# Kernel tuning notes

Measured on AMD Instinct MI355X. Metric: run time of the kernel, lower is better.

## Reference

```python
import jax, jax.numpy as jnp
import numpy as np

B, N, C = 32, 577, 768
H = 12
DH = C // H  # 64
SCALE = DH ** -0.5


def setup_inputs() -> dict:
    key = jax.random.key(0)
    ks = jax.random.split(key, 5)
    x = jax.random.normal(ks[0], (B, N, C), dtype=jnp.float32)
    # Linear params (torch convention: y = x @ W.T + b)
    qkv_w = jax.random.normal(ks[1], (3 * C, C), dtype=jnp.float32) * (C ** -0.5)
    qkv_b = jnp.zeros((3 * C,), dtype=jnp.float32)
    proj_w = jax.random.normal(ks[2], (C, C), dtype=jnp.float32) * (C ** -0.5)
    proj_b = jnp.zeros((C,), dtype=jnp.float32)
    return {"x": x, "qkv_w": qkv_w, "qkv_b": qkv_b, "proj_w": proj_w, "proj_b": proj_b}


def reference(x, qkv_w, qkv_b, proj_w, proj_b):
    b, n, c = x.shape
    qkv = x @ qkv_w.T + qkv_b                       # [B, N, 3C]
    qkv = qkv.reshape(b, n, 3, H, DH).transpose(2, 0, 3, 1, 4)  # [3, B, H, N, DH]
    q, k, v = qkv[0], qkv[1], qkv[2]
    q = q * SCALE
    attn = jnp.einsum('bhnd,bhmd->bhnm', q, k)      # [B, H, N, N]
    # sigmoid -> inverse-sigmoid straight-through rewrite (forward equals logit(sigmoid(attn)))
    sig = jax.nn.sigmoid(attn)
    inv_sig = jnp.log(sig / (1.0 - sig))
    attn_st = attn + jax.lax.stop_gradient(inv_sig - attn)
    p = jax.nn.softmax(attn_st, axis=-1)
    out = jnp.einsum('bhnm,bhmd->bhnd', p, v)       # [B, H, N, DH]
    out = out.transpose(0, 2, 1, 3).reshape(b, n, c)
    return out @ proj_w.T + proj_b
```

## Files before the change

kernel.cpp:

```cpp
#include <hip/hip_runtime.h>

typedef __bf16 bf16;
typedef __attribute__((ext_vector_type(4))) __bf16 bf16x4;
typedef __attribute__((ext_vector_type(8))) __bf16 bf16x8;
typedef __attribute__((ext_vector_type(4))) float f32x4;

#define MFMA_BF16(A_, B_, C_) __builtin_amdgcn_mfma_f32_16x16x32_bf16(A_, B_, C_, 0, 0, 0)

#define BB    32
#define SEQ   577
#define CH    768
#define NH    12
#define DHD   64
#define MROWS (BB * SEQ)
#define NQKV  2304
#define SEQP  584
#define QSCALE 0.1803368801111204f

__device__ __forceinline__ void async_ld16(const bf16* g, bf16* l) {
  __builtin_amdgcn_global_load_lds(
      (const __attribute__((address_space(1))) void*)g,
      (__attribute__((address_space(3))) void*)l, 16, 0, 0);
}

__global__ __launch_bounds__(256) void cvt_bf16(const float* __restrict__ src,
                                                bf16* __restrict__ dst, int n) {
  int idx = (blockIdx.x * 256 + threadIdx.x) * 4;
  if (idx >= n) return;
  float4 v = *(const float4*)(src + idx);
  bf16x4 o = {(bf16)v.x, (bf16)v.y, (bf16)v.z, (bf16)v.w};
  *(bf16x4*)(dst + idx) = o;
}

template <int EPI>
__global__ __launch_bounds__(256, 2)
void gemm_bt(const bf16* __restrict__ A, const bf16* __restrict__ W,
             const float* __restrict__ bias,
             bf16* __restrict__ qrm, bf16* __restrict__ krm, bf16* __restrict__ vt,
             float* __restrict__ out) {
  __shared__ bf16 As[2][128 * 32];
  __shared__ bf16 Bs[2][128 * 32];
  const int tid = threadIdx.x, lane = tid & 63, wid = tid >> 6;
  const int quad = lane >> 4, r15 = lane & 15;
  const int m0 = blockIdx.y * 128, n0 = blockIdx.x * 128;
  const int waveM = wid & 1, waveN = wid >> 1;

  const bf16* aSrc[2];
  const bf16* bSrc[2];
  for (int c = 0; c < 2; ++c) {
    int q = wid * 128 + c * 64 + lane;
    int row = q >> 2;
    int sw = (row ^ (row >> 2)) & 3;
    int kc = (q & 3) ^ sw;
    aSrc[c] = A + (size_t)(m0 + row) * CH + kc * 8;
    bSrc[c] = W + (size_t)(n0 + row) * CH + kc * 8;
  }

  f32x4 acc[4][4];
#pragma unroll
  for (int i = 0; i < 4; ++i)
#pragma unroll
    for (int j = 0; j < 4; ++j) acc[i][j] = (f32x4){0.f, 0.f, 0.f, 0.f};

#define GSTAGE(K0, BUF)                                                   \
  {                                                                       \
    _Pragma("unroll") for (int c = 0; c < 2; ++c) {                       \
      async_ld16(aSrc[c] + (K0), &As[BUF][(wid * 128 + c * 64) * 8]);     \
      async_ld16(bSrc[c] + (K0), &Bs[BUF][(wid * 128 + c * 64) * 8]);     \
    }                                                                     \
  }

#define GCOMPUTE(BUF)                                                     \
  {                                                                       \
    bf16x8 af[4], bfr[4];                                                 \
    _Pragma("unroll") for (int s = 0; s < 4; ++s) {                       \
      int rowA = waveM * 64 + s * 16 + r15;                               \
      int ca = quad ^ ((rowA ^ (rowA >> 2)) & 3);                         \
      af[s] = *(const bf16x8*)(&As[BUF][rowA * 32 + ca * 8]);             \
      int rowB = waveN * 64 + s * 16 + r15;                               \
      int cb = quad ^ ((rowB ^ (rowB >> 2)) & 3);                         \
      bfr[s] = *(const bf16x8*)(&Bs[BUF][rowB * 32 + cb * 8]);            \
    }                                                                     \
    _Pragma("unroll") for (int sm = 0; sm < 4; ++sm)                      \
      _Pragma("unroll") for (int sn = 0; sn < 4; ++sn)                    \
        acc[sm][sn] = MFMA_BF16(af[sm], bfr[sn], acc[sm][sn]);            \
  }

  GSTAGE(0, 0);
  for (int k0 = 0; k0 < CH; k0 += 64) {
    __syncthreads();
    GSTAGE(k0 + 32, 1);
    GCOMPUTE(0);
    __syncthreads();
    if (k0 + 64 < CH) GSTAGE(k0 + 64, 0);
    GCOMPUTE(1);
  }

  if (EPI == 0) {
    int t = (n0 >= 1536) ? 2 : (n0 >= 768 ? 1 : 0);
#pragma unroll
    for (int sn = 0; sn < 4; ++sn) {
      int gn = n0 + waveN * 64 + sn * 16 + r15;
      float bv = bias[gn];
      int col = gn - t * CH;
      int h = col >> 6, d = col & 63;
#pragma unroll
      for (int sm = 0; sm < 4; ++sm) {
        int gmBase = m0 + waveM * 64 + sm * 16 + quad * 4;
#pragma unroll
        for (int r = 0; r < 4; ++r) {
          int gm = gmBase + r;
          if (gm < MROWS) {
            float v = acc[sm][sn][r] + bv;
            if (t == 0) {
              qrm[(size_t)gm * CH + col] = (bf16)(v * QSCALE);
            } else if (t == 1) {
              krm[(size_t)gm * CH + col] = (bf16)v;
            } else {
              int b_ = gm / SEQ;
              int n_ = gm - b_ * SEQ;
              vt[((size_t)(b_ * NH + h) * DHD + d) * SEQP + n_] = (bf16)v;
            }
          }
        }
      }
    }
  } else {
#pragma unroll
    for (int sn = 0; sn < 4; ++sn) {
      int gn = n0 + waveN * 64 + sn * 16 + r15;
      float bv = bias[gn];
#pragma unroll
      for (int sm = 0; sm < 4; ++sm) {
        int gmBase = m0 + waveM * 64 + sm * 16 + quad * 4;
#pragma unroll
        for (int r = 0; r < 4; ++r) {
          int gm = gmBase + r;
          if (gm < MROWS) out[(size_t)gm * CH + gn] = acc[sm][sn][r] + bv;
        }
      }
    }
  }
}

__global__ __launch_bounds__(256, 6)
void attn_kernel(const bf16* __restrict__ qrm, const bf16* __restrict__ krm,
                 const bf16* __restrict__ vt, bf16* __restrict__ ob) {
  __shared__ bf16 Ks[64 * 72];
  __shared__ bf16 Vt[64 * 72];
  const int tid = threadIdx.x, lane = tid & 63, wid = tid >> 6;
  const int quad = lane >> 4, r15 = lane & 15;
  const int qt = blockIdx.x, bh = blockIdx.y;
  const int b_ = bh / NH, h = bh - b_ * NH;
  const bf16* vtb = vt + (size_t)bh * DHD * SEQP;

  int qrow = qt * 64 + wid * 16 + r15;
  if (qrow > SEQ - 1) qrow = SEQ - 1;
  const bf16* qp = qrm + (size_t)(b_ * SEQ + qrow) * CH + h * DHD + quad * 8;
  bf16x8 qf0 = *(const bf16x8*)qp;
  bf16x8 qf1 = *(const bf16x8*)(qp + 32);

  f32x4 oacc[4];
#pragma unroll
  for (int i = 0; i < 4; ++i) oacc[i] = (f32x4){0.f, 0.f, 0.f, 0.f};
  float lrow[4] = {0.f, 0.f, 0.f, 0.f};

  for (int j0 = 0; j0 < SEQ; j0 += 64) {
    __syncthreads();
#pragma unroll
    for (int c = 0; c < 2; ++c) {
      int sid = c * 256 + tid;
      int row = sid >> 3, cc = sid & 7;
      int jr = j0 + row;
      if (jr > SEQ - 1) jr = SEQ - 1;
      *(bf16x8*)(Ks + row * 72 + cc * 8) =
          *(const bf16x8*)(krm + (size_t)(b_ * SEQ + jr) * CH + h * DHD + cc * 8);
      int jst = j0 + cc * 8;
      if (jst > SEQ - 1) jst = SEQ - 1;
      *(bf16x8*)(Vt + row * 72 + cc * 8) = *(const bf16x8*)(vtb + (size_t)row * SEQP + jst);
    }
    __syncthreads();

    f32x4 s[4];
#pragma unroll
    for (int sj = 0; sj < 4; ++sj) {
      bf16x8 kf0 = *(const bf16x8*)(Ks + (sj * 16 + r15) * 72 + quad * 8);
      bf16x8 kf1 = *(const bf16x8*)(Ks + (sj * 16 + r15) * 72 + 32 + quad * 8);
      f32x4 z = (f32x4){0.f, 0.f, 0.f, 0.f};
      s[sj] = MFMA_BF16(qf0, kf0, z);
      s[sj] = MFMA_BF16(qf1, kf1, s[sj]);
    }
#pragma unroll
    for (int sj = 0; sj < 4; ++sj)
      if (j0 + sj * 16 + r15 > SEQ - 1) s[sj] = (f32x4){-1e30f, -1e30f, -1e30f, -1e30f};

#pragma unroll
    for (int sj = 0; sj < 4; ++sj)
#pragma unroll
      for (int r = 0; r < 4; ++r) {
        float e = __builtin_amdgcn_exp2f(s[sj][r]);
        s[sj][r] = e;
        lrow[r] += e;
      }

    __syncthreads();
    bf16* Pw = Ks + wid * (16 * 72);
#pragma unroll
    for (int sj = 0; sj < 4; ++sj)
#pragma unroll
      for (int r = 0; r < 4; ++r)
        Pw[(quad * 4 + r) * 72 + sj * 16 + r15] = (bf16)s[sj][r];
    asm volatile("s_waitcnt lgkmcnt(0)" ::: "memory");

#pragma unroll
    for (int kc = 0; kc < 2; ++kc) {
      bf16x8 pf = *(const bf16x8*)(Pw + r15 * 72 + kc * 32 + quad * 8);
#pragma unroll
      for (int sd = 0; sd < 4; ++sd) {
        bf16x8 vf = *(const bf16x8*)(Vt + (sd * 16 + r15) * 72 + kc * 32 + quad * 8);
        oacc[sd] = MFMA_BF16(pf, vf, oacc[sd]);
      }
    }
  }

#pragma unroll
  for (int r = 0; r < 4; ++r) {
    float rs = lrow[r];
    rs += __shfl_xor(rs, 1);
    rs += __shfl_xor(rs, 2);
    rs += __shfl_xor(rs, 4);
    rs += __shfl_xor(rs, 8);
    lrow[r] = rs;
  }

#pragma unroll
  for (int r = 0; r < 4; ++r) {
    int orow = qt * 64 + wid * 16 + quad * 4 + r;
    if (orow < SEQ) {
      float inv = 1.0f / lrow[r];
      size_t rowoff = ((size_t)(b_ * SEQ + orow)) * CH + h * DHD;
#pragma unroll
      for (int sd = 0; sd < 4; ++sd)
        ob[rowoff + sd * 16 + r15] = (bf16)(oacc[sd][r] * inv);
    }
  }
}

extern "C" void kernel_launch(void* const* d_in, const int* in_sizes, int n_in,
                              void* d_out, int out_size, void* d_ws, size_t ws_size,
                              hipStream_t stream) {
  const float* x      = (const float*)d_in[0];
  const float* qkv_w  = (const float*)d_in[1];
  const float* qkv_b  = (const float*)d_in[2];
  const float* proj_w = (const float*)d_in[3];
  const float* proj_b = (const float*)d_in[4];
  float* out = (float*)d_out;

  char* w = (char*)d_ws;
  bf16* xb  = (bf16*)(w);
  bf16* wqp = (bf16*)(w + 28360704);
  bf16* qrm = (bf16*)(w + 31899648);
  bf16* krm = (bf16*)(w + 60260352);
  bf16* vtb = (bf16*)(w + 88621056);

  cvt_bf16<<<(MROWS * CH / 4 + 255) / 256, 256, 0, stream>>>(x, xb, MROWS * CH);
  cvt_bf16<<<(NQKV * CH / 4 + 255) / 256, 256, 0, stream>>>(qkv_w, wqp, NQKV * CH);

  gemm_bt<0><<<dim3(NQKV / 128, 145), 256, 0, stream>>>(
      xb, wqp, qkv_b, qrm, krm, vtb, nullptr);

  attn_kernel<<<dim3(10, BB * NH), 256, 0, stream>>>(qrm, krm, vtb, xb);

  cvt_bf16<<<(CH * CH / 4 + 255) / 256, 256, 0, stream>>>(proj_w, wqp, CH * CH);

  gemm_bt<1><<<dim3(CH / 128, 145), 256, 0, stream>>>(
      xb, wqp, proj_b, nullptr, nullptr, nullptr, out);
}
```

Baseline: 397.2 us.

## Enlarge GEMM tiles to 256x256 with 512 threads and XCD-aware block remap

```diff
diff --git a/kernel.cpp b/kernel.cpp
--- a/kernel.cpp
+++ b/kernel.cpp
@@ -17,6 +17,8 @@
 #define SEQP  584
 #define QSCALE 0.1803368801111204f
 
+#define NT (CH / 64)
+
 __device__ __forceinline__ void async_ld16(const bf16* g, bf16* l) {
   __builtin_amdgcn_global_load_lds(
       (const __attribute__((address_space(1))) void*)g,
@@ -33,88 +35,105 @@
 }
 
 template <int EPI>
-__global__ __launch_bounds__(256, 2)
+__global__ __launch_bounds__(512, 2)
 void gemm_bt(const bf16* __restrict__ A, const bf16* __restrict__ W,
              const float* __restrict__ bias,
              bf16* __restrict__ qrm, bf16* __restrict__ krm, bf16* __restrict__ vt,
              float* __restrict__ out) {
-  __shared__ bf16 As[2][128 * 32];
-  __shared__ bf16 Bs[2][128 * 32];
+  __shared__ bf16 As[2][2][256 * 32];
+  __shared__ bf16 Bs[2][2][256 * 32];
   const int tid = threadIdx.x, lane = tid & 63, wid = tid >> 6;
   const int quad = lane >> 4, r15 = lane & 15;
-  const int m0 = blockIdx.y * 128, n0 = blockIdx.x * 128;
-  const int waveM = wid & 1, waveN = wid >> 1;
-
-  const bf16* aSrc[2];
-  const bf16* bSrc[2];
-  for (int c = 0; c < 2; ++c) {
-    int q = wid * 128 + c * 64 + lane;
-    int row = q >> 2;
-    int sw = (row ^ (row >> 2)) & 3;
-    int kc = (q & 3) ^ sw;
-    aSrc[c] = A + (size_t)(m0 + row) * CH + kc * 8;
-    bSrc[c] = W + (size_t)(n0 + row) * CH + kc * 8;
-  }
-
-  f32x4 acc[4][4];
-#pragma unroll
-  for (int i = 0; i < 4; ++i)
+
+  const int nbx = (int)gridDim.x;
+  const int nwg = nbx * (int)gridDim.y;
+  int bid = (int)blockIdx.y * nbx + (int)blockIdx.x;
+  int q8 = nwg >> 3, r8 = nwg & 7;
+  int xcd = bid & 7, sub = bid >> 3;
+  int wg = (xcd < r8 ? xcd * (q8 + 1) : r8 * (q8 + 1) + (xcd - r8) * q8) + sub;
+  const int m0 = (wg / nbx) * 256, n0 = (wg % nbx) * 256;
+
+  const int rm = (wid >> 2) * 128;
+  const int rn = (wid & 3) * 64;
+
+  int aOff[4], bOff[4];
+#pragma unroll
+  for (int i = 0; i < 4; ++i) {
+    int slot = i * 512 + tid;
+    int row = (slot >> 2) & 255, ks = slot >> 10, pc2 = slot & 3;
+    int gc2 = pc2 ^ ((row ^ (row >> 2)) & 3);
+    aOff[i] = (m0 + row) * CH + ks * 32 + gc2 * 8;
+    bOff[i] = (n0 + row) * CH + ks * 32 + gc2 * 8;
+  }
+
+  f32x4 acc[8][4];
+#pragma unroll
+  for (int i = 0; i < 8; ++i)
 #pragma unroll
     for (int j = 0; j < 4; ++j) acc[i][j] = (f32x4){0.f, 0.f, 0.f, 0.f};
 
-#define GSTAGE(K0, BUF)                                                   \
-  {                                                                       \
-    _Pragma("unroll") for (int c = 0; c < 2; ++c) {                       \
-      async_ld16(aSrc[c] + (K0), &As[BUF][(wid * 128 + c * 64) * 8]);     \
-      async_ld16(bSrc[c] + (K0), &Bs[BUF][(wid * 128 + c * 64) * 8]);     \
-    }                                                                     \
-  }
-
-#define GCOMPUTE(BUF)                                                     \
-  {                                                                       \
-    bf16x8 af[4], bfr[4];                                                 \
-    _Pragma("unroll") for (int s = 0; s < 4; ++s) {                       \
-      int rowA = waveM * 64 + s * 16 + r15;                               \
-      int ca = quad ^ ((rowA ^ (rowA >> 2)) & 3);                         \
-      af[s] = *(const bf16x8*)(&As[BUF][rowA * 32 + ca * 8]);             \
-      int rowB = waveN * 64 + s * 16 + r15;                               \
-      int cb = quad ^ ((rowB ^ (rowB >> 2)) & 3);                         \
-      bfr[s] = *(const bf16x8*)(&Bs[BUF][rowB * 32 + cb * 8]);            \
-    }                                                                     \
-    _Pragma("unroll") for (int sm = 0; sm < 4; ++sm)                      \
-      _Pragma("unroll") for (int sn = 0; sn < 4; ++sn)                    \
-        acc[sm][sn] = MFMA_BF16(af[sm], bfr[sn], acc[sm][sn]);            \
+#define GSTAGE(K0, BUF)                                                        \
+  {                                                                            \
+    _Pragma("unroll") for (int i = 0; i < 4; ++i) {                            \
+      async_ld16(A + aOff[i] + (K0), &As[BUF][0][(i * 512 + tid) * 8]);        \
+      async_ld16(W + bOff[i] + (K0), &Bs[BUF][0][(i * 512 + tid) * 8]);        \
+    }                                                                          \
+  }
+
+#define GCOMPUTE(BUF)                                                          \
+  {                                                                            \
+    bf16x8 bfr[4][2];                                                          \
+    _Pragma("unroll") for (int sn = 0; sn < 4; ++sn) {                         \
+      int fr = rn + sn * 16 + r15;                                             \
+      int pc2 = quad ^ ((fr ^ (fr >> 2)) & 3);                                 \
+      bfr[sn][0] = *(const bf16x8*)(&Bs[BUF][0][fr * 32 + pc2 * 8]);           \
+      bfr[sn][1] = *(const bf16x8*)(&Bs[BUF][1][fr * 32 + pc2 * 8]);           \
+    }                                                                          \
+    _Pragma("unroll") for (int sp = 0; sp < 4; ++sp) {                         \
+      bf16x8 af[2][2];                                                         \
+      _Pragma("unroll") for (int s2 = 0; s2 < 2; ++s2) {                       \
+        int fr = rm + (sp * 2 + s2) * 16 + r15;                                \
+        int pc2 = quad ^ ((fr ^ (fr >> 2)) & 3);                               \
+        af[s2][0] = *(const bf16x8*)(&As[BUF][0][fr * 32 + pc2 * 8]);          \
+        af[s2][1] = *(const bf16x8*)(&As[BUF][1][fr * 32 + pc2 * 8]);          \
+      }                                                                        \
+      _Pragma("unroll") for (int s2 = 0; s2 < 2; ++s2)                         \
+        _Pragma("unroll") for (int sn = 0; sn < 4; ++sn) {                     \
+          acc[sp * 2 + s2][sn] =                                               \
+              MFMA_BF16(af[s2][0], bfr[sn][0], acc[sp * 2 + s2][sn]);          \
+          acc[sp * 2 + s2][sn] =                                               \
+              MFMA_BF16(af[s2][1], bfr[sn][1], acc[sp * 2 + s2][sn]);          \
+        }                                                                      \
+    }                                                                          \
   }
 
   GSTAGE(0, 0);
-  for (int k0 = 0; k0 < CH; k0 += 64) {
-    __syncthreads();
-    GSTAGE(k0 + 32, 1);
-    GCOMPUTE(0);
-    __syncthreads();
-    if (k0 + 64 < CH) GSTAGE(k0 + 64, 0);
-    GCOMPUTE(1);
+  for (int t = 0; t < NT; ++t) {
+    int buf = t & 1;
+    __syncthreads();
+    if (t + 1 < NT) GSTAGE((t + 1) * 64, buf ^ 1);
+    GCOMPUTE(buf);
   }
 
   if (EPI == 0) {
-    int t = (n0 >= 1536) ? 2 : (n0 >= 768 ? 1 : 0);
+    int tcl = (n0 >= 1536) ? 2 : (n0 >= 768 ? 1 : 0);
 #pragma unroll
     for (int sn = 0; sn < 4; ++sn) {
-      int gn = n0 + waveN * 64 + sn * 16 + r15;
+      int gn = n0 + rn + sn * 16 + r15;
       float bv = bias[gn];
-      int col = gn - t * CH;
+      int col = gn - tcl * CH;
       int h = col >> 6, d = col & 63;
 #pragma unroll
-      for (int sm = 0; sm < 4; ++sm) {
-        int gmBase = m0 + waveM * 64 + sm * 16 + quad * 4;
+      for (int sm = 0; sm < 8; ++sm) {
+        int gmBase = m0 + rm + sm * 16 + quad * 4;
 #pragma unroll
         for (int r = 0; r < 4; ++r) {
           int gm = gmBase + r;
           if (gm < MROWS) {
             float v = acc[sm][sn][r] + bv;
-            if (t == 0) {
+            if (tcl == 0) {
               qrm[(size_t)gm * CH + col] = (bf16)(v * QSCALE);
-            } else if (t == 1) {
+            } else if (tcl == 1) {
               krm[(size_t)gm * CH + col] = (bf16)v;
             } else {
               int b_ = gm / SEQ;
@@ -128,11 +147,11 @@
   } else {
 #pragma unroll
     for (int sn = 0; sn < 4; ++sn) {
-      int gn = n0 + waveN * 64 + sn * 16 + r15;
+      int gn = n0 + rn + sn * 16 + r15;
       float bv = bias[gn];
 #pragma unroll
-      for (int sm = 0; sm < 4; ++sm) {
-        int gmBase = m0 + waveM * 64 + sm * 16 + quad * 4;
+      for (int sm = 0; sm < 8; ++sm) {
+        int gmBase = m0 + rm + sm * 16 + quad * 4;
 #pragma unroll
         for (int r = 0; r < 4; ++r) {
           int gm = gmBase + r;
@@ -266,13 +285,13 @@
   cvt_bf16<<<(MROWS * CH / 4 + 255) / 256, 256, 0, stream>>>(x, xb, MROWS * CH);
   cvt_bf16<<<(NQKV * CH / 4 + 255) / 256, 256, 0, stream>>>(qkv_w, wqp, NQKV * CH);
 
-  gemm_bt<0><<<dim3(NQKV / 128, 145), 256, 0, stream>>>(
+  gemm_bt<0><<<dim3(NQKV / 256, 73), 512, 0, stream>>>(
       xb, wqp, qkv_b, qrm, krm, vtb, nullptr);
 
   attn_kernel<<<dim3(10, BB * NH), 256, 0, stream>>>(qrm, krm, vtb, xb);
 
   cvt_bf16<<<(CH * CH / 4 + 255) / 256, 256, 0, stream>>>(proj_w, wqp, CH * CH);
 
-  gemm_bt<1><<<dim3(CH / 128, 145), 256, 0, stream>>>(
+  gemm_bt<1><<<dim3(CH / 256, 73), 512, 0, stream>>>(
       xb, wqp, proj_b, nullptr, nullptr, nullptr, out);
 }
```

New measurement: 415.9 us. 1.05x slower.

## Load K and V fragments directly from global in attention, drop shared staging

Applied to the files above, without the earlier changes.

```diff
diff --git a/kernel.cpp b/kernel.cpp
--- a/kernel.cpp
+++ b/kernel.cpp
@@ -30,6 +30,15 @@
   float4 v = *(const float4*)(src + idx);
   bf16x4 o = {(bf16)v.x, (bf16)v.y, (bf16)v.z, (bf16)v.w};
   *(bf16x4*)(dst + idx) = o;
+}
+
+__global__ __launch_bounds__(256) void pad_v(bf16* __restrict__ vt) {
+  int r = blockIdx.x * 256 + threadIdx.x;
+  if (r < BB * NH * DHD) {
+    bf16* p = vt + (size_t)r * SEQP + SEQ;
+#pragma unroll
+    for (int i = 0; i < 7; ++i) p[i] = (bf16)0.f;
+  }
 }
 
 template <int EPI>
@@ -146,13 +155,13 @@
 __global__ __launch_bounds__(256, 6)
 void attn_kernel(const bf16* __restrict__ qrm, const bf16* __restrict__ krm,
                  const bf16* __restrict__ vt, bf16* __restrict__ ob) {
-  __shared__ bf16 Ks[64 * 72];
-  __shared__ bf16 Vt[64 * 72];
+  __shared__ bf16 Ps[4][16 * 72];
   const int tid = threadIdx.x, lane = tid & 63, wid = tid >> 6;
   const int quad = lane >> 4, r15 = lane & 15;
   const int qt = blockIdx.x, bh = blockIdx.y;
   const int b_ = bh / NH, h = bh - b_ * NH;
   const bf16* vtb = vt + (size_t)bh * DHD * SEQP;
+  const bf16* kb = krm + (size_t)b_ * SEQ * CH + h * DHD;
 
   int qrow = qt * 64 + wid * 16 + r15;
   if (qrow > SEQ - 1) qrow = SEQ - 1;
@@ -165,27 +174,17 @@
   for (int i = 0; i < 4; ++i) oacc[i] = (f32x4){0.f, 0.f, 0.f, 0.f};
   float lrow[4] = {0.f, 0.f, 0.f, 0.f};
 
+  bf16* Pw = Ps[wid];
+
   for (int j0 = 0; j0 < SEQ; j0 += 64) {
-    __syncthreads();
-#pragma unroll
-    for (int c = 0; c < 2; ++c) {
-      int sid = c * 256 + tid;
-      int row = sid >> 3, cc = sid & 7;
-      int jr = j0 + row;
+    f32x4 s[4];
+#pragma unroll
+    for (int sj = 0; sj < 4; ++sj) {
+      int jr = j0 + sj * 16 + r15;
       if (jr > SEQ - 1) jr = SEQ - 1;
-      *(bf16x8*)(Ks + row * 72 + cc * 8) =
-          *(const bf16x8*)(krm + (size_t)(b_ * SEQ + jr) * CH + h * DHD + cc * 8);
-      int jst = j0 + cc * 8;
-      if (jst > SEQ - 1) jst = SEQ - 1;
-      *(bf16x8*)(Vt + row * 72 + cc * 8) = *(const bf16x8*)(vtb + (size_t)row * SEQP + jst);
-    }
-    __syncthreads();
-
-    f32x4 s[4];
-#pragma unroll
-    for (int sj = 0; sj < 4; ++sj) {
-      bf16x8 kf0 = *(const bf16x8*)(Ks + (sj * 16 + r15) * 72 + quad * 8);
-      bf16x8 kf1 = *(const bf16x8*)(Ks + (sj * 16 + r15) * 72 + 32 + quad * 8);
+      const bf16* kp = kb + (size_t)jr * CH + quad * 8;
+      bf16x8 kf0 = *(const bf16x8*)kp;
+      bf16x8 kf1 = *(const bf16x8*)(kp + 32);
       f32x4 z = (f32x4){0.f, 0.f, 0.f, 0.f};
       s[sj] = MFMA_BF16(qf0, kf0, z);
       s[sj] = MFMA_BF16(qf1, kf1, s[sj]);
@@ -203,8 +202,6 @@
         lrow[r] += e;
       }
 
-    __syncthreads();
-    bf16* Pw = Ks + wid * (16 * 72);
 #pragma unroll
     for (int sj = 0; sj < 4; ++sj)
 #pragma unroll
@@ -215,9 +212,11 @@
 #pragma unroll
     for (int kc = 0; kc < 2; ++kc) {
       bf16x8 pf = *(const bf16x8*)(Pw + r15 * 72 + kc * 32 + quad * 8);
+      int jc = j0 + kc * 32 + quad * 8;
+      if (jc > SEQ - 1) jc = SEQ - 1 - 7;
 #pragma unroll
       for (int sd = 0; sd < 4; ++sd) {
-        bf16x8 vf = *(const bf16x8*)(Vt + (sd * 16 + r15) * 72 + kc * 32 + quad * 8);
+        bf16x8 vf = *(const bf16x8*)(vtb + (size_t)(sd * 16 + r15) * SEQP + jc);
         oacc[sd] = MFMA_BF16(pf, vf, oacc[sd]);
       }
     }
@@ -265,6 +264,7 @@
 
   cvt_bf16<<<(MROWS * CH / 4 + 255) / 256, 256, 0, stream>>>(x, xb, MROWS * CH);
   cvt_bf16<<<(NQKV * CH / 4 + 255) / 256, 256, 0, stream>>>(qkv_w, wqp, NQKV * CH);
+  pad_v<<<(BB * NH * DHD + 255) / 256, 256, 0, stream>>>(vtb);
 
   gemm_bt<0><<<dim3(NQKV / 128, 145), 256, 0, stream>>>(
       xb, wqp, qkv_b, qrm, krm, vtb, nullptr);
```

Measured after the change: 511.3 us. 28.7% more time.
